# Kernel tuning notes

Hardware: AMD Instinct MI355X
Metric: run time of the kernel (lower is better)

Reference implementation:

```python
import jax, jax.numpy as jnp
import numpy as np

M = 12          # persons per frame
K = 2           # partition channels from conv1da (1024 = 2*512)
D = 512         # GCN channel dim / LSTM hidden
C_IN = 4096     # backbone feature dim
NUM_CLASSES = 8


def setup_inputs() -> dict:
    key = jax.random.key(0)
    ks = jax.random.split(key, 8)
    N, T = 16, 32
    NT = N * T
    base_out = jax.random.normal(ks[0], (NT, M, C_IN), dtype=jnp.float32)
    dist = jax.random.uniform(ks[1], (N, T, 3, K, M, M), dtype=jnp.float32)
    # conv1da: Conv1d(4096 -> 1024, k=1, bias=False) == matmul with [1024, 4096]
    w_a = jax.random.normal(ks[2], (K * D, C_IN), dtype=jnp.float32) * 0.02
    # LSTM(512, 512, 1): torch gate order i, f, g, o
    s = 1.0 / np.sqrt(D)
    w_ih = jax.random.uniform(ks[3], (4 * D, D), minval=-s, maxval=s, dtype=jnp.float32)
    w_hh = jax.random.uniform(ks[4], (4 * D, D), minval=-s, maxval=s, dtype=jnp.float32)
    b_ih = jax.random.uniform(ks[5], (4 * D,), minval=-s, maxval=s, dtype=jnp.float32)
    b_hh = jax.random.uniform(ks[6], (4 * D,), minval=-s, maxval=s, dtype=jnp.float32)
    # gclassifier: Linear(512 -> num_classes)
    w_cls = jax.random.normal(ks[7], (NUM_CLASSES, D), dtype=jnp.float32) * 0.01
    b_cls = jnp.zeros((NUM_CLASSES,), dtype=jnp.float32)
    return {"base_out": base_out, "dist": dist, "w_a": w_a,
            "w_ih": w_ih, "w_hh": w_hh, "b_ih": b_ih, "b_hh": b_hh,
            "w_cls": w_cls, "b_cls": b_cls, "n_videos": N}


def reference(base_out, dist, w_a, w_ih, w_hh, b_ih, b_hh, w_cls, b_cls, n_videos):
    NT = base_out.shape[0]
    N = n_videos
    T = NT // N
    # conv1da (1x1 conv, no bias): [NT, M, 4096] -> [NT, K*D, M] -> [NT, K, D, M]
    node1 = jnp.einsum('nmc,oc->nom', base_out, w_a).reshape(NT, K, D, M)
    # fused three-way adjacency aggregation: node1a + node1b + node1c
    A = (dist[:, :, 2] + dist[:, :, 1] + dist[:, :, 0]).reshape(NT, K, M, M)
    node = jnp.einsum('nkcv,nkvw->ncw', node1, A)  # [NT, D, M]
    node = jax.nn.relu(node)
    # AdaptiveAvgPool1d(1) over the M persons
    pooled = node.mean(axis=2)                      # [NT, D]
    seq = pooled.reshape(N, T, D)
    # torch nn.LSTM default batch_first=False: iterates over axis 0 (N), batch=T
    def step(carry, x_t):
        h, c = carry
        g = x_t @ w_ih.T + b_ih + h @ w_hh.T + b_hh  # [T, 4D]
        i, f, gg, o = jnp.split(g, 4, axis=-1)
        c = jax.nn.sigmoid(f) * c + jax.nn.sigmoid(i) * jnp.tanh(gg)
        h = jax.nn.sigmoid(o) * jnp.tanh(c)
        return (h, c), h
    h0 = jnp.zeros((T, D), dtype=seq.dtype)
    c0 = jnp.zeros((T, D), dtype=seq.dtype)
    _, hs = jax.lax.scan(step, (h0, c0), seq)       # [N, T, D]
    last = hs[:, -1, :]                              # video_feat[:, -1, :]
    return last @ w_cls.T + b_cls                    # [N, num_classes]
```

## Files before the change

### kernel.cpp

```cpp
#include <hip/hip_runtime.h>
#include <math.h>

#define MM 12
#define KK 2
#define DD 512
#define CIN 4096
#define NCLS 8
#define NV 16
#define TT 32

typedef unsigned long long u64;

#define PART_F   0
#define POOLED_F 786432
#define GX_F     794624
#define SLOT_F   827392

__global__ __launch_bounds__(256) void k_gemm(const float* __restrict__ w_a,
                                              const float* __restrict__ base_out,
                                              float* __restrict__ part) {
    const int ks = blockIdx.x;
    const int ot = blockIdx.y;
    const int jt = blockIdx.z;
    const int tid = threadIdx.x;

    __shared__ __align__(16) float As[16][68];
    __shared__ __align__(16) float Bs[16][68];

    const int to = tid & 15;
    const int tj = tid >> 4;

    const int lrow = tid >> 2;
    const int lq   = tid & 3;
    const size_t a_base = (size_t)(ot * 64 + lrow) * CIN;
    const int j_stage = jt * 64 + lrow;
    const int n_stage = j_stage / 12;
    const int m_stage = j_stage - n_stage * 12;
    const size_t b_base = (size_t)((n_stage * TT + 31) * MM + m_stage) * CIN;

    float acc[4][4];
#pragma unroll
    for (int i = 0; i < 4; ++i)
#pragma unroll
        for (int jj = 0; jj < 4; ++jj) acc[i][jj] = 0.f;

    int cc0 = ks * 1024;
    for (int it = 0; it < 64; ++it, cc0 += 16) {
        float4 av = *(const float4*)&w_a[a_base + cc0 + lq * 4];
        float4 bv = *(const float4*)&base_out[b_base + cc0 + lq * 4];
        __syncthreads();
        As[lq * 4 + 0][lrow] = av.x; As[lq * 4 + 1][lrow] = av.y;
        As[lq * 4 + 2][lrow] = av.z; As[lq * 4 + 3][lrow] = av.w;
        Bs[lq * 4 + 0][lrow] = bv.x; Bs[lq * 4 + 1][lrow] = bv.y;
        Bs[lq * 4 + 2][lrow] = bv.z; Bs[lq * 4 + 3][lrow] = bv.w;
        __syncthreads();
#pragma unroll
        for (int cl = 0; cl < 16; ++cl) {
            float4 a = *(const float4*)&As[cl][to * 4];
            float4 b = *(const float4*)&Bs[cl][tj * 4];
            acc[0][0] += a.x * b.x; acc[0][1] += a.x * b.y; acc[0][2] += a.x * b.z; acc[0][3] += a.x * b.w;
            acc[1][0] += a.y * b.x; acc[1][1] += a.y * b.y; acc[1][2] += a.y * b.z; acc[1][3] += a.y * b.w;
            acc[2][0] += a.z * b.x; acc[2][1] += a.z * b.y; acc[2][2] += a.z * b.z; acc[2][3] += a.z * b.w;
            acc[3][0] += a.w * b.x; acc[3][1] += a.w * b.y; acc[3][2] += a.w * b.z; acc[3][3] += a.w * b.w;
        }
    }

    const int o_base = ot * 64 + to * 4;
#pragma unroll
    for (int jj = 0; jj < 4; ++jj) {
        const int j = jt * 64 + tj * 4 + jj;
        float4 v = make_float4(acc[0][jj], acc[1][jj], acc[2][jj], acc[3][jj]);
        *(float4*)&part[(size_t)ks * (192 * 1024) + (size_t)j * 1024 + o_base] = v;
    }
}

__global__ __launch_bounds__(256) void k_pool(const float* __restrict__ part,
                                              const float* __restrict__ dist,
                                              float* __restrict__ pooled) {
    const int n = blockIdx.x;
    const int tid = threadIdx.x;
    __shared__ float Asum[KK][MM][MM];

    const size_t dbase = (size_t)(n * TT + 31) * (3 * KK * MM * MM);
    for (int f = tid; f < KK * MM * MM; f += 256) {
        const int k = f / (MM * MM);
        const int rem = f - k * (MM * MM);
        float s = dist[dbase + 0 * (KK * MM * MM) + k * (MM * MM) + rem]
                + dist[dbase + 1 * (KK * MM * MM) + k * (MM * MM) + rem]
                + dist[dbase + 2 * (KK * MM * MM) + k * (MM * MM) + rem];
        Asum[k][rem / MM][rem % MM] = s;
    }
    __syncthreads();

    for (int c = tid; c < DD; c += 256) {
        float nd[KK][MM];
#pragma unroll
        for (int k = 0; k < KK; ++k)
#pragma unroll
            for (int v = 0; v < MM; ++v) {
                const size_t off = (size_t)(n * MM + v) * 1024 + (k * DD + c);
                nd[k][v] = part[off] + part[off + 1 * (192 * 1024)]
                         + part[off + 2 * (192 * 1024)] + part[off + 3 * (192 * 1024)];
            }
        float accm = 0.f;
#pragma unroll
        for (int w = 0; w < MM; ++w) {
            float sw = 0.f;
#pragma unroll
            for (int k = 0; k < KK; ++k)
#pragma unroll
                for (int v = 0; v < MM; ++v) sw += nd[k][v] * Asum[k][v][w];
            accm += fmaxf(sw, 0.f);
        }
        pooled[n * DD + c] = accm * (1.f / 12.f);
    }
}

__global__ __launch_bounds__(256) void k_gx(const float* __restrict__ pooled,
                                            const float* __restrict__ w_ih,
                                            const float* __restrict__ b_ih,
                                            const float* __restrict__ b_hh,
                                            float* __restrict__ gx) {
    const int wg = blockIdx.x;
    const int tid = threadIdx.x;
    __shared__ __align__(16) float w_s[16][516];

    for (int f = tid; f < 16 * DD; f += 256) {
        const int r = f >> 9, col = f & 511;
        w_s[r][col] = w_ih[(size_t)(wg * 16 + r) * DD + col];
    }
    __syncthreads();

    const int r = tid & 15;
    const int n = tid >> 4;
    const float4* wr = (const float4*)&w_s[r][0];
    const float4* pv = (const float4*)(pooled + n * DD);
    float acc = 0.f;
#pragma unroll 8
    for (int q = 0; q < DD / 4; ++q) {
        float4 a = wr[q], b = pv[q];
        acc += a.x * b.x + a.y * b.y + a.z * b.z + a.w * b.w;
    }
    const int row = wg * 16 + r;
    gx[n * (4 * DD) + row] = acc + b_ih[row] + b_hh[row];
}

__global__ __launch_bounds__(256) void k_lstm(const float* __restrict__ w_hh,
                                              const float* __restrict__ gx,
                                              const float* __restrict__ w_cls,
                                              const float* __restrict__ b_cls,
                                              u64* __restrict__ slots,
                                              float* __restrict__ out) {
    const int wg = blockIdx.x;
    const int tid = threadIdx.x;

    __shared__ __align__(16) float whh_s[16][516];
    __shared__ __align__(16) float h_s[DD];
    __shared__ float dot_s[16];

    for (int f = tid; f < 16 * DD; f += 256) {
        const int rl = f >> 9, col = f & 511;
        const int gate = rl >> 2, dl = rl & 3;
        whh_s[rl][col] = w_hh[(size_t)(gate * DD + wg * 4 + dl) * DD + col];
    }

    float c_reg = 0.f;
    const int rl = tid >> 4;
    const int lj = tid & 15;

    for (int s = 0; s < NV; ++s) {
        if (s == 0) {
            for (int d = tid; d < DD; d += 256) h_s[d] = 0.f;
        } else {
            const u64* slot = slots + (size_t)(s - 1) * DD;
            for (int d = tid; d < DD; d += 256) {
                u64 v;
                do {
                    v = __hip_atomic_load(&slot[d], __ATOMIC_RELAXED, __HIP_MEMORY_SCOPE_AGENT);
                } while ((unsigned)(v & 0xffffffffull) != (unsigned)s);
                union { unsigned u; float f; } cv; cv.u = (unsigned)(v >> 32);
                h_s[d] = cv.f;
            }
        }
        __syncthreads();

        float p = 0.f;
        const float4* wrow = (const float4*)&whh_s[rl][0];
        const float4* hv4 = (const float4*)h_s;
#pragma unroll
        for (int q = 0; q < 8; ++q) {
            float4 wv = wrow[lj + 16 * q];
            float4 hv = hv4[lj + 16 * q];
            p += wv.x * hv.x + wv.y * hv.y + wv.z * hv.z + wv.w * hv.w;
        }
#pragma unroll
        for (int off = 8; off; off >>= 1) p += __shfl_down(p, off, 16);
        if (lj == 0) dot_s[rl] = p;
        __syncthreads();

        if (tid < 4) {
            const int dg = wg * 4 + tid;
            const float* gxs = gx + s * (4 * DD);
            const float pi = gxs[0 * DD + dg] + dot_s[0 + tid];
            const float pf = gxs[1 * DD + dg] + dot_s[4 + tid];
            const float pg = gxs[2 * DD + dg] + dot_s[8 + tid];
            const float po = gxs[3 * DD + dg] + dot_s[12 + tid];
            const float si = 1.f / (1.f + expf(-pi));
            const float sf = 1.f / (1.f + expf(-pf));
            const float so = 1.f / (1.f + expf(-po));
            c_reg = sf * c_reg + si * tanhf(pg);
            const float hn = so * tanhf(c_reg);
            union { float f; unsigned u; } hv_; hv_.f = hn;
            const u64 pack = ((u64)hv_.u << 32) | (u64)(unsigned)(s + 1);
            __hip_atomic_store(&slots[(size_t)s * DD + dg], pack,
                               __ATOMIC_RELAXED, __HIP_MEMORY_SCOPE_AGENT);
        }
    }

    if (wg == 0) {
        __syncthreads();
        for (int f = tid; f < NV * DD; f += 256) {
            const int ss = f >> 9, d = f & 511;
            u64 v;
            do {
                v = __hip_atomic_load(&slots[(size_t)ss * DD + d],
                                      __ATOMIC_RELAXED, __HIP_MEMORY_SCOPE_AGENT);
            } while ((unsigned)(v & 0xffffffffull) != (unsigned)(ss + 1));
            union { unsigned u; float f; } cv; cv.u = (unsigned)(v >> 32);
            whh_s[ss][d] = cv.f;
        }
        __syncthreads();
        if (tid < NV * NCLS) {
            const int n = tid >> 3, cl = tid & 7;
            const float4* hv = (const float4*)&whh_s[n][0];
            const float4* wv = (const float4*)(w_cls + (size_t)cl * DD);
            float acc = b_cls[cl];
#pragma unroll 8
            for (int q = 0; q < DD / 4; ++q) {
                float4 a = hv[q], b = wv[q];
                acc += a.x * b.x + a.y * b.y + a.z * b.z + a.w * b.w;
            }
            out[tid] = acc;
        }
    }
}

extern "C" void kernel_launch(void* const* d_in, const int* in_sizes, int n_in,
                              void* d_out, int out_size, void* d_ws, size_t ws_size,
                              hipStream_t stream) {
    const float* base_out = (const float*)d_in[0];
    const float* dist     = (const float*)d_in[1];
    const float* w_a      = (const float*)d_in[2];
    const float* w_ih     = (const float*)d_in[3];
    const float* w_hh     = (const float*)d_in[4];
    const float* b_ih     = (const float*)d_in[5];
    const float* b_hh     = (const float*)d_in[6];
    const float* w_cls    = (const float*)d_in[7];
    const float* b_cls    = (const float*)d_in[8];
    float* out = (float*)d_out;

    float* ws = (float*)d_ws;
    float* part   = ws + PART_F;
    float* pooled = ws + POOLED_F;
    float* gx     = ws + GX_F;
    u64*   slots  = (u64*)(ws + SLOT_F);

    k_gemm<<<dim3(4, 16, 3), 256, 0, stream>>>(w_a, base_out, part);
    k_pool<<<dim3(16), 256, 0, stream>>>(part, dist, pooled);
    k_gx<<<dim3(128), 256, 0, stream>>>(pooled, w_ih, b_ih, b_hh, gx);
    k_lstm<<<dim3(128), 256, 0, stream>>>(w_hh, gx, w_cls, b_cls, slots, out);
}
```

Before: 286.5 us.

## Fuse all stages into one persistent kernel with split-bf16 MFMA GEMM

Replaces the four launches (GEMM, pool, input gates, LSTM) with a single 256-workgroup kernel that uses global tag flags as grid barriers between stages. The GEMM now runs on bf16 MFMA with a hi/lo split of each fp32 operand (three products) to stay near fp32 accuracy. The LSTM keeps its hidden-state slots replicated eight times to cut polling contention, and keeps input-gate results in LDS. Risks: the grid barriers assume every workgroup is resident at once (deadlock otherwise), the slots reuse the part region that is no longer needed, and the split-bf16 path loses some precision.

```diff
diff --git a/kernel.cpp b/kernel.cpp
--- a/kernel.cpp
+++ b/kernel.cpp
@@ -10,263 +10,319 @@
 #define TT 32
 
 typedef unsigned long long u64;
+typedef __attribute__((ext_vector_type(8))) __bf16 bf16x8;
+typedef __attribute__((ext_vector_type(4))) float f32x4;
 
 #define PART_F   0
 #define POOLED_F 786432
-#define GX_F     794624
-#define SLOT_F   827392
-
-__global__ __launch_bounds__(256) void k_gemm(const float* __restrict__ w_a,
-                                              const float* __restrict__ base_out,
-                                              float* __restrict__ part) {
-    const int ks = blockIdx.x;
-    const int ot = blockIdx.y;
-    const int jt = blockIdx.z;
-    const int tid = threadIdx.x;
-
-    __shared__ __align__(16) float As[16][68];
-    __shared__ __align__(16) float Bs[16][68];
-
-    const int to = tid & 15;
-    const int tj = tid >> 4;
-
-    const int lrow = tid >> 2;
-    const int lq   = tid & 3;
-    const size_t a_base = (size_t)(ot * 64 + lrow) * CIN;
-    const int j_stage = jt * 64 + lrow;
-    const int n_stage = j_stage / 12;
-    const int m_stage = j_stage - n_stage * 12;
-    const size_t b_base = (size_t)((n_stage * TT + 31) * MM + m_stage) * CIN;
-
-    float acc[4][4];
-#pragma unroll
-    for (int i = 0; i < 4; ++i)
-#pragma unroll
-        for (int jj = 0; jj < 4; ++jj) acc[i][jj] = 0.f;
-
-    int cc0 = ks * 1024;
-    for (int it = 0; it < 64; ++it, cc0 += 16) {
-        float4 av = *(const float4*)&w_a[a_base + cc0 + lq * 4];
-        float4 bv = *(const float4*)&base_out[b_base + cc0 + lq * 4];
-        __syncthreads();
-        As[lq * 4 + 0][lrow] = av.x; As[lq * 4 + 1][lrow] = av.y;
-        As[lq * 4 + 2][lrow] = av.z; As[lq * 4 + 3][lrow] = av.w;
-        Bs[lq * 4 + 0][lrow] = bv.x; Bs[lq * 4 + 1][lrow] = bv.y;
-        Bs[lq * 4 + 2][lrow] = bv.z; Bs[lq * 4 + 3][lrow] = bv.w;
-        __syncthreads();
-#pragma unroll
-        for (int cl = 0; cl < 16; ++cl) {
-            float4 a = *(const float4*)&As[cl][to * 4];
-            float4 b = *(const float4*)&Bs[cl][tj * 4];
-            acc[0][0] += a.x * b.x; acc[0][1] += a.x * b.y; acc[0][2] += a.x * b.z; acc[0][3] += a.x * b.w;
-            acc[1][0] += a.y * b.x; acc[1][1] += a.y * b.y; acc[1][2] += a.y * b.z; acc[1][3] += a.y * b.w;
-            acc[2][0] += a.z * b.x; acc[2][1] += a.z * b.y; acc[2][2] += a.z * b.z; acc[2][3] += a.z * b.w;
-            acc[3][0] += a.w * b.x; acc[3][1] += a.w * b.y; acc[3][2] += a.w * b.z; acc[3][3] += a.w * b.w;
+#define TAGA_F   794624
+#define TAGB_F   794880
+#define PART_KS_STRIDE (192 * 1024)
+
+#define MFMA_BF16(A, B, C) __builtin_amdgcn_mfma_f32_16x16x32_bf16((A), (B), (C), 0, 0, 0)
+
+__global__ __launch_bounds__(256, 1) void k_fused(
+    const float* __restrict__ base_out, const float* __restrict__ dist,
+    const float* __restrict__ w_a, const float* __restrict__ w_ih,
+    const float* __restrict__ w_hh, const float* __restrict__ b_ih,
+    const float* __restrict__ b_hh, const float* __restrict__ w_cls,
+    const float* __restrict__ b_cls,
+    float* __restrict__ part, float* __restrict__ pooled,
+    unsigned* __restrict__ tagA, unsigned* __restrict__ tagB,
+    u64* __restrict__ slots, float* __restrict__ out)
+{
+  const int wg = blockIdx.x;
+  const int tid = threadIdx.x;
+
+  __shared__ __align__(16) unsigned short Ah[16 * 40], Al[16 * 40];
+  __shared__ __align__(16) unsigned short Bh[192 * 40], Bl[192 * 40];
+  __shared__ __align__(16) float whh_s[16][516];
+  __shared__ __align__(16) float wih_s[16][516];
+  __shared__ __align__(16) float pooled_s[16][520];
+  __shared__ float gx_s[16][20];
+  __shared__ __align__(16) float h_s[DD];
+  __shared__ float dot_s[16];
+  __shared__ float Asum_s[KK * MM * MM];
+
+  {
+    const int ks = wg >> 6, ot = wg & 63;
+    const int cc0 = ks * 1024;
+    const int wave = tid >> 6, lane = tid & 63;
+    const int jf0 = wave * 3;
+
+    const int sq = tid & 7;
+    const int sr = tid >> 3;
+    unsigned boff[6];
+#pragma unroll
+    for (int rep = 0; rep < 6; ++rep) {
+      const int j = sr + 32 * rep;
+      const int n = j / 12, m = j - n * 12;
+      boff[rep] = (unsigned)(((n * TT + 31) * MM + m) * CIN + cc0 + sq * 4);
+    }
+    const bool aact = tid < 128;
+    unsigned aoff = aact ? (unsigned)((ot * 16 + (tid >> 3)) * CIN + cc0 + sq * 4) : 0u;
+
+    f32x4 acc0 = {0.f, 0.f, 0.f, 0.f}, acc1 = acc0, acc2 = acc0;
+
+    float4 pa, pb[6];
+    if (aact) pa = *(const float4*)&w_a[aoff];
+#pragma unroll
+    for (int rep = 0; rep < 6; ++rep) pb[rep] = *(const float4*)&base_out[boff[rep]];
+
+    for (int st = 0; st < 32; ++st) {
+      __syncthreads();
+      if (aact) {
+        const int idx = (tid >> 3) * 40 + sq * 4;
+        unsigned ux = __float_as_uint(pa.x), uy = __float_as_uint(pa.y);
+        unsigned uz = __float_as_uint(pa.z), uw = __float_as_uint(pa.w);
+        *(uint2*)&Ah[idx] = make_uint2((ux >> 16) | (uy & 0xFFFF0000u),
+                                       (uz >> 16) | (uw & 0xFFFF0000u));
+        unsigned lx = __float_as_uint(pa.x - __uint_as_float(ux & 0xFFFF0000u));
+        unsigned ly = __float_as_uint(pa.y - __uint_as_float(uy & 0xFFFF0000u));
+        unsigned lz = __float_as_uint(pa.z - __uint_as_float(uz & 0xFFFF0000u));
+        unsigned lw = __float_as_uint(pa.w - __uint_as_float(uw & 0xFFFF0000u));
+        *(uint2*)&Al[idx] = make_uint2((lx >> 16) | (ly & 0xFFFF0000u),
+                                       (lz >> 16) | (lw & 0xFFFF0000u));
+      }
+#pragma unroll
+      for (int rep = 0; rep < 6; ++rep) {
+        const int idx = (sr + 32 * rep) * 40 + sq * 4;
+        unsigned ux = __float_as_uint(pb[rep].x), uy = __float_as_uint(pb[rep].y);
+        unsigned uz = __float_as_uint(pb[rep].z), uw = __float_as_uint(pb[rep].w);
+        *(uint2*)&Bh[idx] = make_uint2((ux >> 16) | (uy & 0xFFFF0000u),
+                                       (uz >> 16) | (uw & 0xFFFF0000u));
+        unsigned lx = __float_as_uint(pb[rep].x - __uint_as_float(ux & 0xFFFF0000u));
+        unsigned ly = __float_as_uint(pb[rep].y - __uint_as_float(uy & 0xFFFF0000u));
+        unsigned lz = __float_as_uint(pb[rep].z - __uint_as_float(uz & 0xFFFF0000u));
+        unsigned lw = __float_as_uint(pb[rep].w - __uint_as_float(uw & 0xFFFF0000u));
+        *(uint2*)&Bl[idx] = make_uint2((lx >> 16) | (ly & 0xFFFF0000u),
+                                       (lz >> 16) | (lw & 0xFFFF0000u));
+      }
+      __syncthreads();
+      if (st < 31) {
+        aoff += 32;
+        if (aact) pa = *(const float4*)&w_a[aoff];
+#pragma unroll
+        for (int rep = 0; rep < 6; ++rep) {
+          boff[rep] += 32;
+          pb[rep] = *(const float4*)&base_out[boff[rep]];
         }
-    }
-
-    const int o_base = ot * 64 + to * 4;
-#pragma unroll
-    for (int jj = 0; jj < 4; ++jj) {
-        const int j = jt * 64 + tj * 4 + jj;
-        float4 v = make_float4(acc[0][jj], acc[1][jj], acc[2][jj], acc[3][jj]);
-        *(float4*)&part[(size_t)ks * (192 * 1024) + (size_t)j * 1024 + o_base] = v;
-    }
-}
-
-__global__ __launch_bounds__(256) void k_pool(const float* __restrict__ part,
-                                              const float* __restrict__ dist,
-                                              float* __restrict__ pooled) {
-    const int n = blockIdx.x;
-    const int tid = threadIdx.x;
-    __shared__ float Asum[KK][MM][MM];
-
-    const size_t dbase = (size_t)(n * TT + 31) * (3 * KK * MM * MM);
-    for (int f = tid; f < KK * MM * MM; f += 256) {
-        const int k = f / (MM * MM);
-        const int rem = f - k * (MM * MM);
-        float s = dist[dbase + 0 * (KK * MM * MM) + k * (MM * MM) + rem]
-                + dist[dbase + 1 * (KK * MM * MM) + k * (MM * MM) + rem]
-                + dist[dbase + 2 * (KK * MM * MM) + k * (MM * MM) + rem];
-        Asum[k][rem / MM][rem % MM] = s;
-    }
-    __syncthreads();
-
-    for (int c = tid; c < DD; c += 256) {
-        float nd[KK][MM];
+      }
+      const int koff = (lane >> 4) * 8;
+      const int fra = (lane & 15) * 40 + koff;
+      bf16x8 oh = *(const bf16x8*)&Ah[fra];
+      bf16x8 ol = *(const bf16x8*)&Al[fra];
+      {
+        const int r0 = ((jf0 + 0) * 16 + (lane & 15)) * 40 + koff;
+        bf16x8 jh = *(const bf16x8*)&Bh[r0], jl = *(const bf16x8*)&Bl[r0];
+        acc0 = MFMA_BF16(jh, oh, acc0);
+        acc0 = MFMA_BF16(jh, ol, acc0);
+        acc0 = MFMA_BF16(jl, oh, acc0);
+      }
+      {
+        const int r1 = ((jf0 + 1) * 16 + (lane & 15)) * 40 + koff;
+        bf16x8 jh = *(const bf16x8*)&Bh[r1], jl = *(const bf16x8*)&Bl[r1];
+        acc1 = MFMA_BF16(jh, oh, acc1);
+        acc1 = MFMA_BF16(jh, ol, acc1);
+        acc1 = MFMA_BF16(jl, oh, acc1);
+      }
+      {
+        const int r2 = ((jf0 + 2) * 16 + (lane & 15)) * 40 + koff;
+        bf16x8 jh = *(const bf16x8*)&Bh[r2], jl = *(const bf16x8*)&Bl[r2];
+        acc2 = MFMA_BF16(jh, oh, acc2);
+        acc2 = MFMA_BF16(jh, ol, acc2);
+        acc2 = MFMA_BF16(jl, oh, acc2);
+      }
+    }
+    const int o = ot * 16 + (lane & 15);
+    const int jr = (lane >> 4) * 4;
+#pragma unroll
+    for (int r = 0; r < 4; ++r) {
+      part[((size_t)ks * 192 + (jf0 + 0) * 16 + jr + r) * 1024 + o] = acc0[r];
+      part[((size_t)ks * 192 + (jf0 + 1) * 16 + jr + r) * 1024 + o] = acc1[r];
+      part[((size_t)ks * 192 + (jf0 + 2) * 16 + jr + r) * 1024 + o] = acc2[r];
+    }
+    __syncthreads();
+    if (tid == 0)
+      __hip_atomic_store(&tagA[wg], 1u, __ATOMIC_RELEASE, __HIP_MEMORY_SCOPE_AGENT);
+  }
+
+  if (wg < 128) {
+    for (int f = tid; f < 16 * DD; f += 256) {
+      const int rl = f >> 9, col = f & 511;
+      const int row = (rl >> 2) * DD + wg * 4 + (rl & 3);
+      whh_s[rl][col] = w_hh[(size_t)row * DD + col];
+      wih_s[rl][col] = w_ih[(size_t)row * DD + col];
+    }
+  }
+
+  while (__hip_atomic_load(&tagA[tid], __ATOMIC_RELAXED, __HIP_MEMORY_SCOPE_AGENT) != 1u) {}
+  __syncthreads();
+  (void)__hip_atomic_load(&tagA[0], __ATOMIC_ACQUIRE, __HIP_MEMORY_SCOPE_AGENT);
+
+  {
+    const int n = wg >> 4, cb = (wg & 15) * 32;
+    const unsigned dbase = (unsigned)((n * TT + 31) * (3 * KK * MM * MM));
+    for (int f = tid; f < KK * MM * MM; f += 256)
+      Asum_s[f] = dist[dbase + f] + dist[dbase + KK * MM * MM + f]
+                + dist[dbase + 2 * KK * MM * MM + f];
+    __syncthreads();
+    if (tid < 32) {
+      const int c = cb + tid;
+      float nd[KK][MM];
+#pragma unroll
+      for (int k = 0; k < KK; ++k)
+#pragma unroll
+        for (int v = 0; v < MM; ++v) {
+          const size_t off = (size_t)(n * MM + v) * 1024 + k * DD + c;
+          nd[k][v] = part[off] + part[off + PART_KS_STRIDE]
+                   + part[off + 2 * PART_KS_STRIDE] + part[off + 3 * PART_KS_STRIDE];
+        }
+      float accm = 0.f;
+#pragma unroll
+      for (int w = 0; w < MM; ++w) {
+        float sw = 0.f;
 #pragma unroll
         for (int k = 0; k < KK; ++k)
 #pragma unroll
-            for (int v = 0; v < MM; ++v) {
-                const size_t off = (size_t)(n * MM + v) * 1024 + (k * DD + c);
-                nd[k][v] = part[off] + part[off + 1 * (192 * 1024)]
-                         + part[off + 2 * (192 * 1024)] + part[off + 3 * (192 * 1024)];
-            }
-        float accm = 0.f;
-#pragma unroll
-        for (int w = 0; w < MM; ++w) {
-            float sw = 0.f;
-#pragma unroll
-            for (int k = 0; k < KK; ++k)
-#pragma unroll
-                for (int v = 0; v < MM; ++v) sw += nd[k][v] * Asum[k][v][w];
-            accm += fmaxf(sw, 0.f);
-        }
-        pooled[n * DD + c] = accm * (1.f / 12.f);
-    }
-}
-
-__global__ __launch_bounds__(256) void k_gx(const float* __restrict__ pooled,
-                                            const float* __restrict__ w_ih,
-                                            const float* __restrict__ b_ih,
-                                            const float* __restrict__ b_hh,
-                                            float* __restrict__ gx) {
-    const int wg = blockIdx.x;
-    const int tid = threadIdx.x;
-    __shared__ __align__(16) float w_s[16][516];
-
-    for (int f = tid; f < 16 * DD; f += 256) {
-        const int r = f >> 9, col = f & 511;
-        w_s[r][col] = w_ih[(size_t)(wg * 16 + r) * DD + col];
-    }
-    __syncthreads();
-
-    const int r = tid & 15;
-    const int n = tid >> 4;
-    const float4* wr = (const float4*)&w_s[r][0];
-    const float4* pv = (const float4*)(pooled + n * DD);
-    float acc = 0.f;
+          for (int v = 0; v < MM; ++v) sw += nd[k][v] * Asum_s[(k * MM + v) * MM + w];
+        accm += fmaxf(sw, 0.f);
+      }
+      pooled[n * DD + c] = accm * (1.f / 12.f);
+    }
+    __syncthreads();
+    if (tid == 0)
+      __hip_atomic_store(&tagB[wg], 1u, __ATOMIC_RELEASE, __HIP_MEMORY_SCOPE_AGENT);
+  }
+  if (wg >= 128) return;
+
+  while (__hip_atomic_load(&tagB[tid], __ATOMIC_RELAXED, __HIP_MEMORY_SCOPE_AGENT) != 1u) {}
+  __syncthreads();
+  (void)__hip_atomic_load(&tagB[0], __ATOMIC_ACQUIRE, __HIP_MEMORY_SCOPE_AGENT);
+
+  for (int f = tid; f < NV * DD; f += 256) pooled_s[f >> 9][f & 511] = pooled[f];
+  __syncthreads();
+  {
+    const int rl = tid & 15, n = tid >> 4;
+    const float4* wr = (const float4*)&wih_s[rl][0];
+    const float4* pv = (const float4*)&pooled_s[n][0];
+    float a = 0.f;
 #pragma unroll 8
     for (int q = 0; q < DD / 4; ++q) {
-        float4 a = wr[q], b = pv[q];
-        acc += a.x * b.x + a.y * b.y + a.z * b.z + a.w * b.w;
-    }
-    const int row = wg * 16 + r;
-    gx[n * (4 * DD) + row] = acc + b_ih[row] + b_hh[row];
-}
-
-__global__ __launch_bounds__(256) void k_lstm(const float* __restrict__ w_hh,
-                                              const float* __restrict__ gx,
-                                              const float* __restrict__ w_cls,
-                                              const float* __restrict__ b_cls,
-                                              u64* __restrict__ slots,
-                                              float* __restrict__ out) {
-    const int wg = blockIdx.x;
-    const int tid = threadIdx.x;
-
-    __shared__ __align__(16) float whh_s[16][516];
-    __shared__ __align__(16) float h_s[DD];
-    __shared__ float dot_s[16];
-
-    for (int f = tid; f < 16 * DD; f += 256) {
-        const int rl = f >> 9, col = f & 511;
-        const int gate = rl >> 2, dl = rl & 3;
-        whh_s[rl][col] = w_hh[(size_t)(gate * DD + wg * 4 + dl) * DD + col];
-    }
-
+      float4 x = wr[q], y = pv[q];
+      a += x.x * y.x + x.y * y.y + x.z * y.z + x.w * y.w;
+    }
+    const int row = (rl >> 2) * DD + wg * 4 + (rl & 3);
+    gx_s[n][rl] = a + b_ih[row] + b_hh[row];
+  }
+  __syncthreads();
+
+  {
     float c_reg = 0.f;
-    const int rl = tid >> 4;
+    const int r = tid >> 4;
     const int lj = tid & 15;
 
     for (int s = 0; s < NV; ++s) {
-        if (s == 0) {
-            for (int d = tid; d < DD; d += 256) h_s[d] = 0.f;
-        } else {
-            const u64* slot = slots + (size_t)(s - 1) * DD;
-            for (int d = tid; d < DD; d += 256) {
-                u64 v;
-                do {
-                    v = __hip_atomic_load(&slot[d], __ATOMIC_RELAXED, __HIP_MEMORY_SCOPE_AGENT);
-                } while ((unsigned)(v & 0xffffffffull) != (unsigned)s);
-                union { unsigned u; float f; } cv; cv.u = (unsigned)(v >> 32);
-                h_s[d] = cv.f;
-            }
-        }
-        __syncthreads();
-
-        float p = 0.f;
-        const float4* wrow = (const float4*)&whh_s[rl][0];
-        const float4* hv4 = (const float4*)h_s;
-#pragma unroll
-        for (int q = 0; q < 8; ++q) {
-            float4 wv = wrow[lj + 16 * q];
-            float4 hv = hv4[lj + 16 * q];
-            p += wv.x * hv.x + wv.y * hv.y + wv.z * hv.z + wv.w * hv.w;
-        }
-#pragma unroll
-        for (int off = 8; off; off >>= 1) p += __shfl_down(p, off, 16);
-        if (lj == 0) dot_s[rl] = p;
-        __syncthreads();
-
-        if (tid < 4) {
-            const int dg = wg * 4 + tid;
-            const float* gxs = gx + s * (4 * DD);
-            const float pi = gxs[0 * DD + dg] + dot_s[0 + tid];
-            const float pf = gxs[1 * DD + dg] + dot_s[4 + tid];
-            const float pg = gxs[2 * DD + dg] + dot_s[8 + tid];
-            const float po = gxs[3 * DD + dg] + dot_s[12 + tid];
-            const float si = 1.f / (1.f + expf(-pi));
-            const float sf = 1.f / (1.f + expf(-pf));
-            const float so = 1.f / (1.f + expf(-po));
-            c_reg = sf * c_reg + si * tanhf(pg);
-            const float hn = so * tanhf(c_reg);
-            union { float f; unsigned u; } hv_; hv_.f = hn;
-            const u64 pack = ((u64)hv_.u << 32) | (u64)(unsigned)(s + 1);
-            __hip_atomic_store(&slots[(size_t)s * DD + dg], pack,
-                               __ATOMIC_RELAXED, __HIP_MEMORY_SCOPE_AGENT);
-        }
-    }
-
-    if (wg == 0) {
-        __syncthreads();
-        for (int f = tid; f < NV * DD; f += 256) {
-            const int ss = f >> 9, d = f & 511;
-            u64 v;
-            do {
-                v = __hip_atomic_load(&slots[(size_t)ss * DD + d],
-                                      __ATOMIC_RELAXED, __HIP_MEMORY_SCOPE_AGENT);
-            } while ((unsigned)(v & 0xffffffffull) != (unsigned)(ss + 1));
-            union { unsigned u; float f; } cv; cv.u = (unsigned)(v >> 32);
-            whh_s[ss][d] = cv.f;
-        }
-        __syncthreads();
-        if (tid < NV * NCLS) {
-            const int n = tid >> 3, cl = tid & 7;
-            const float4* hv = (const float4*)&whh_s[n][0];
-            const float4* wv = (const float4*)(w_cls + (size_t)cl * DD);
-            float acc = b_cls[cl];
+      if (s == 0) {
+        h_s[tid] = 0.f; h_s[tid + 256] = 0.f;
+      } else {
+        const u64* slot = slots + ((size_t)(wg & 7) * NV + (s - 1)) * DD;
+        u64 v0 = __hip_atomic_load(&slot[tid], __ATOMIC_RELAXED, __HIP_MEMORY_SCOPE_AGENT);
+        u64 v1 = __hip_atomic_load(&slot[tid + 256], __ATOMIC_RELAXED, __HIP_MEMORY_SCOPE_AGENT);
+        while ((unsigned)v0 != (unsigned)s)
+          v0 = __hip_atomic_load(&slot[tid], __ATOMIC_RELAXED, __HIP_MEMORY_SCOPE_AGENT);
+        while ((unsigned)v1 != (unsigned)s)
+          v1 = __hip_atomic_load(&slot[tid + 256], __ATOMIC_RELAXED, __HIP_MEMORY_SCOPE_AGENT);
+        h_s[tid] = __uint_as_float((unsigned)(v0 >> 32));
+        h_s[tid + 256] = __uint_as_float((unsigned)(v1 >> 32));
+      }
+      __syncthreads();
+
+      float p = 0.f;
+      const float4* wrow = (const float4*)&whh_s[r][0];
+      const float4* hv4 = (const float4*)h_s;
+#pragma unroll
+      for (int q = 0; q < 8; ++q) {
+        float4 wv = wrow[lj + 16 * q];
+        float4 hv = hv4[lj + 16 * q];
+        p += wv.x * hv.x + wv.y * hv.y + wv.z * hv.z + wv.w * hv.w;
+      }
+#pragma unroll
+      for (int off = 8; off; off >>= 1) p += __shfl_down(p, off, 16);
+      if (lj == 0) dot_s[r] = p;
+      __syncthreads();
+
+      u64 pack = 0;
+      if (tid < 4) {
+        const float pi = gx_s[s][tid]      + dot_s[tid];
+        const float pf = gx_s[s][4 + tid]  + dot_s[4 + tid];
+        const float pg = gx_s[s][8 + tid]  + dot_s[8 + tid];
+        const float po = gx_s[s][12 + tid] + dot_s[12 + tid];
+        const float si = 1.f / (1.f + expf(-pi));
+        const float sf = 1.f / (1.f + expf(-pf));
+        const float so = 1.f / (1.f + expf(-po));
+        c_reg = sf * c_reg + si * tanhf(pg);
+        const float hn = so * tanhf(c_reg);
+        pack = ((u64)__float_as_uint(hn) << 32) | (u64)(unsigned)(s + 1);
+      }
+      if (tid < 32) {
+        u64 pk = __shfl(pack, tid & 3, 64);
+        const int rep = tid >> 2;
+        __hip_atomic_store(&slots[((size_t)rep * NV + s) * DD + wg * 4 + (tid & 3)], pk,
+                           __ATOMIC_RELAXED, __HIP_MEMORY_SCOPE_AGENT);
+      }
+    }
+  }
+
+  if (wg == 0) {
+    __syncthreads();
+    for (int f = tid; f < NV * DD; f += 256) {
+      const int ss = f >> 9, d = f & 511;
+      u64 v = __hip_atomic_load(&slots[(size_t)ss * DD + d],
+                                __ATOMIC_RELAXED, __HIP_MEMORY_SCOPE_AGENT);
+      while ((unsigned)v != (unsigned)(ss + 1))
+        v = __hip_atomic_load(&slots[(size_t)ss * DD + d],
+                              __ATOMIC_RELAXED, __HIP_MEMORY_SCOPE_AGENT);
+      pooled_s[ss][d] = __uint_as_float((unsigned)(v >> 32));
+    }
+    __syncthreads();
+    if (tid < NV * NCLS) {
+      const int n = tid >> 3, cl = tid & 7;
+      const float4* hv = (const float4*)&pooled_s[n][0];
+      const float4* wv = (const float4*)(w_cls + (size_t)cl * DD);
+      float a = b_cls[cl];
 #pragma unroll 8
-            for (int q = 0; q < DD / 4; ++q) {
-                float4 a = hv[q], b = wv[q];
-                acc += a.x * b.x + a.y * b.y + a.z * b.z + a.w * b.w;
-            }
-            out[tid] = acc;
-        }
-    }
+      for (int q = 0; q < DD / 4; ++q) {
+        float4 x = hv[q], y = wv[q];
+        a += x.x * y.x + x.y * y.y + x.z * y.z + x.w * y.w;
+      }
+      out[tid] = a;
+    }
+  }
 }
 
 extern "C" void kernel_launch(void* const* d_in, const int* in_sizes, int n_in,
                               void* d_out, int out_size, void* d_ws, size_t ws_size,
                               hipStream_t stream) {
-    const float* base_out = (const float*)d_in[0];
-    const float* dist     = (const float*)d_in[1];
-    const float* w_a      = (const float*)d_in[2];
-    const float* w_ih     = (const float*)d_in[3];
-    const float* w_hh     = (const float*)d_in[4];
-    const float* b_ih     = (const float*)d_in[5];
-    const float* b_hh     = (const float*)d_in[6];
-    const float* w_cls    = (const float*)d_in[7];
-    const float* b_cls    = (const float*)d_in[8];
-    float* out = (float*)d_out;
-
-    float* ws = (float*)d_ws;
-    float* part   = ws + PART_F;
-    float* pooled = ws + POOLED_F;
-    float* gx     = ws + GX_F;
-    u64*   slots  = (u64*)(ws + SLOT_F);
-
-    k_gemm<<<dim3(4, 16, 3), 256, 0, stream>>>(w_a, base_out, part);
-    k_pool<<<dim3(16), 256, 0, stream>>>(part, dist, pooled);
-    k_gx<<<dim3(128), 256, 0, stream>>>(pooled, w_ih, b_ih, b_hh, gx);
-    k_lstm<<<dim3(128), 256, 0, stream>>>(w_hh, gx, w_cls, b_cls, slots, out);
+  const float* base_out = (const float*)d_in[0];
+  const float* dist     = (const float*)d_in[1];
+  const float* w_a      = (const float*)d_in[2];
+  const float* w_ih     = (const float*)d_in[3];
+  const float* w_hh     = (const float*)d_in[4];
+  const float* b_ih     = (const float*)d_in[5];
+  const float* b_hh     = (const float*)d_in[6];
+  const float* w_cls    = (const float*)d_in[7];
+  const float* b_cls    = (const float*)d_in[8];
+  float* out = (float*)d_out;
+
+  float* ws = (float*)d_ws;
+  float* part   = ws + PART_F;
+  float* pooled = ws + POOLED_F;
+  unsigned* tagA = (unsigned*)(ws + TAGA_F);
+  unsigned* tagB = (unsigned*)(ws + TAGB_F);
+  u64* slots = (u64*)ws;
+
+  k_fused<<<dim3(256), 256, 0, stream>>>(base_out, dist, w_a, w_ih, w_hh,
+                                         b_ih, b_hh, w_cls, b_cls,
+                                         part, pooled, tagA, tagB, slots, out);
 }
```

After: 273.2 us. 1.05x faster.
